# Kernel optimization log

Hardware: AMD Instinct MI355X
Metric: run time of the kernel (lower is better)

The kernel has to match this reference:

```python
import jax, jax.numpy as jnp
import numpy as np

TOP_K = 2  # moe_top_k


def setup_inputs() -> dict:
    key = jax.random.key(0)
    k0, k1, k2, k3 = jax.random.split(key, 4)
    SL, BS, H, F, E = 2048, 4, 1024, 1024, 8
    x = jax.random.normal(k0, (SL, BS, H), dtype=jnp.float32)
    w_router = jax.random.normal(k1, (H, E), dtype=jnp.float32) * 0.02
    w1 = jax.random.normal(k2, (E, H, F), dtype=jnp.float32) * 0.02  # per-expert map weights
    w2 = jax.random.normal(k3, (E, F, H), dtype=jnp.float32) * 0.02  # per-expert reduce weights
    return {"x": x, "w_router": w_router, "w1": w1, "w2": w2}


def reference(x, w_router, w1, w2):
    # dMoA forward: router -> dropless dispatch -> per-expert map GEMM ->
    # per-expert reduce GEMM -> expert-weighted combine. Dropless = no capacity
    # dropping, so a dense all-experts compute + per-token selection is exactly
    # equivalent in math to the sort/gather/grouped-GEMM/scatter pipeline.
    sl, bs, h = x.shape
    E = w1.shape[0]
    xt = x.reshape(-1, h)  # [T, H], T = sl*bs
    T = xt.shape[0]

    # LearnedRouter: softmax over expert logits, then top-k weights/indices
    scores = jax.nn.softmax(xt @ w_router, axis=-1)       # [T, E]
    expert_weights, top_experts = jax.lax.top_k(scores, TOP_K)  # [T, K]

    # load-balancing loss (router.loss): E * sum_e f_e * p_e
    onehot = jax.nn.one_hot(top_experts, E, dtype=xt.dtype)  # [T, K, E]
    tokens_frac = onehot.sum(axis=(0, 1)) / (T * TOP_K)      # f_e
    probs_mean = scores.mean(axis=0)                         # p_e
    loss = E * jnp.sum(tokens_frac * probs_mean)

    # map: per-expert linear H->F, select the top-k experts' outputs per token
    y_all = jnp.einsum('th,ehf->tef', xt, w1)                 # [T, E, F]
    h_tk = jnp.take_along_axis(y_all, top_experts[:, :, None], axis=1)  # [T, K, F]

    # reduce: weighted scatter-combine, then per-expert linear F->H
    hw = jnp.einsum('tke,tk,tkf->tef', onehot, expert_weights, h_tk)  # [T, E, F]
    out = jnp.einsum('tef,efh->th', hw, w2)                   # [T, H]
    return out.reshape(sl, bs, h), loss
```

## Files before the change

### kernel.cpp

```cpp
#include <hip/hip_runtime.h>
#include <hip/hip_bf16.h>
#include <stdint.h>


#define HD 1024
#define FD 1024
#define EN 8

typedef __attribute__((ext_vector_type(8))) short bf16x8;
typedef __attribute__((ext_vector_type(4))) float f32x4;

__device__ __forceinline__ void gload16(const void* g, void* l) {
    __builtin_amdgcn_global_load_lds(
        (const __attribute__((address_space(1))) unsigned int*)g,
        (__attribute__((address_space(3))) unsigned int*)l, 16, 0, 0);
}

__device__ __forceinline__ ushort f2bf(float v) {
    __hip_bfloat16 h = __float2bfloat16(v);
    return *(ushort*)&h;
}
__device__ __forceinline__ float bf2f(ushort u) {
    unsigned int w = ((unsigned int)u) << 16;
    float f; __builtin_memcpy(&f, &w, 4); return f;
}

__global__ __launch_bounds__(256) void router_kernel(
    const float* __restrict__ x, const float* __restrict__ wrt,
    ushort* __restrict__ xb,
    int* __restrict__ top_e, float* __restrict__ top_w,
    int* __restrict__ counts, float* __restrict__ probsum)
{
    __shared__ int   cnt_s[EN];
    __shared__ float ps_s[EN];
    int tid = threadIdx.x;
    if (tid < EN) { cnt_s[tid] = 0; ps_s[tid] = 0.f; }
    __syncthreads();

    int wid = tid >> 6, lane = tid & 63;
    int t = blockIdx.x * 4 + wid;
    const float4* xr4 = (const float4*)(x + (size_t)t * HD);
    ushort4* xbo = (ushort4*)(xb + (size_t)t * HD);
    float acc[EN];
#pragma unroll
    for (int e = 0; e < EN; e++) acc[e] = 0.f;
#pragma unroll
    for (int it = 0; it < 4; it++) {
        float4 xv = xr4[it * 64 + lane];
        ushort4 o; o.x = f2bf(xv.x); o.y = f2bf(xv.y); o.z = f2bf(xv.z); o.w = f2bf(xv.w);
        xbo[it * 64 + lane] = o;
        int h0 = it * 256 + lane * 4;
        float xs[4] = {xv.x, xv.y, xv.z, xv.w};
#pragma unroll
        for (int j = 0; j < 4; j++) {
            const float4* wp = (const float4*)(wrt + (size_t)(h0 + j) * EN);
            float4 wa = wp[0], wb = wp[1];
            acc[0] += xs[j] * wa.x; acc[1] += xs[j] * wa.y;
            acc[2] += xs[j] * wa.z; acc[3] += xs[j] * wa.w;
            acc[4] += xs[j] * wb.x; acc[5] += xs[j] * wb.y;
            acc[6] += xs[j] * wb.z; acc[7] += xs[j] * wb.w;
        }
    }
#pragma unroll
    for (int off = 32; off >= 1; off >>= 1) {
#pragma unroll
        for (int e = 0; e < EN; e++) acc[e] += __shfl_xor(acc[e], off, 64);
    }
    if (lane == 0) {
        float m = acc[0];
#pragma unroll
        for (int e = 1; e < EN; e++) m = fmaxf(m, acc[e]);
        float p[EN], s = 0.f;
#pragma unroll
        for (int e = 0; e < EN; e++) { p[e] = expf(acc[e] - m); s += p[e]; }
        float inv = 1.f / s;
#pragma unroll
        for (int e = 0; e < EN; e++) p[e] *= inv;
        int e0 = 0;
#pragma unroll
        for (int e = 1; e < EN; e++) if (p[e] > p[e0]) e0 = e;
        int e1 = (e0 == 0) ? 1 : 0;
#pragma unroll
        for (int e = 0; e < EN; e++) {
            if (e == e0) continue;
            if (p[e] > p[e1]) e1 = e;
        }
        top_e[t * 2] = e0;  top_e[t * 2 + 1] = e1;
        top_w[t * 2] = p[e0]; top_w[t * 2 + 1] = p[e1];
        atomicAdd(&cnt_s[e0], 1); atomicAdd(&cnt_s[e1], 1);
#pragma unroll
        for (int e = 0; e < EN; e++) atomicAdd(&ps_s[e], p[e]);
    }
    __syncthreads();
    if (tid < EN) {
        atomicAdd(&counts[tid], cnt_s[tid]);
        atomicAdd(&probsum[tid], ps_s[tid]);
    }
}

__global__ void prep_kernel(const int* __restrict__ counts,
                            const float* __restrict__ probsum,
                            int* __restrict__ offs, float* __restrict__ loss_out)
{
    int off = 0; float loss = 0.f;
    for (int e = 0; e < EN; e++) {
        offs[e] = off;
        off += counts[e];
        loss += ((float)counts[e] / 16384.f) * (probsum[e] / 8192.f);
    }
    offs[EN] = off;
    *loss_out = 8.f * loss;
}

__global__ __launch_bounds__(256) void dispatch_kernel(
    const int* __restrict__ top_e, const float* __restrict__ top_w,
    const int* __restrict__ offs, int* __restrict__ cursor,
    int* __restrict__ tok_list, float* __restrict__ w_list)
{
    int t = blockIdx.x * 256 + threadIdx.x;
    int lane = threadIdx.x & 63;
#pragma unroll
    for (int k = 0; k < 2; k++) {
        int e = top_e[t * 2 + k];
        int idx = 0;
#pragma unroll
        for (int ex = 0; ex < EN; ex++) {
            unsigned long long m = __ballot(e == ex);
            if (e == ex) {
                int cnt = __popcll(m);
                int leader = __ffsll(m) - 1;
                int pos = 0;
                if (lane == leader) pos = atomicAdd(&cursor[ex * 16], cnt);
                pos = __shfl(pos, leader, 64);
                int rank = __popcll(m & ((1ull << lane) - 1ull));
                idx = offs[ex] + pos + rank;
            }
        }
        tok_list[idx] = t * 2 + k;
        w_list[idx] = top_w[t * 2 + k];
    }
}

__global__ __launch_bounds__(256) void transpose_conv_kernel(
    const float* __restrict__ w1, const float* __restrict__ w2,
    ushort* __restrict__ w1b, ushort* __restrict__ w2b)
{
    __shared__ float tile[32][33];
    int bid = blockIdx.x;
    const float* in; ushort* outp;
    if (bid >= 8192) { in = w2; outp = w2b; bid -= 8192; }
    else             { in = w1; outp = w1b; }
    int e  = bid >> 10;
    int t2 = bid & 1023;
    int tb = t2 >> 5;
    int ta = t2 & 31;
    const float* pin = in + ((size_t)e << 20);
    ushort* pout = outp + ((size_t)e << 20);
    int tx = threadIdx.x & 31, ty = threadIdx.x >> 5;
#pragma unroll
    for (int j = 0; j < 4; j++)
        tile[ty + j * 8][tx] = pin[(size_t)(ta * 32 + ty + j * 8) * 1024 + tb * 32 + tx];
    __syncthreads();
#pragma unroll
    for (int j = 0; j < 4; j++)
        pout[(size_t)(tb * 32 + ty + j * 8) * 1024 + ta * 32 + tx] =
            f2bf(tile[tx][ty + j * 8]);
}


__global__ __launch_bounds__(512, 2) void map_gemm(
    const ushort* __restrict__ xb, const ushort* __restrict__ w1b,
    ushort* __restrict__ hbuf,
    const int* __restrict__ tok_list, const float* __restrict__ w_list,
    const int* __restrict__ offs)
{
    __shared__ __align__(16) short lA[2][256][64];
    __shared__ __align__(16) short lB[2][256][64];
    __shared__ int   tok_s[256];
    __shared__ float wt_s[256];

    int g = blockIdx.x;
    int e = g & 7, q = g >> 3, nb = q & 3, rb = q >> 2;
    int base = offs[e], cnt = offs[e + 1] - base;
    int row0 = rb << 8;
    if (row0 >= cnt) return;
    int rem = cnt - row0;
    int tid = threadIdx.x;
    if (tid < 256) {
        int r = row0 + tid; if (r > cnt - 1) r = cnt - 1;
        tok_s[tid] = tok_list[base + r];
        wt_s[tid]  = w_list[base + r];
    }
    __syncthreads();

    int lane = tid & 63, w = tid >> 6;
    int wm = w >> 2, wn = w & 3;
    int w32 = w * 32;
    int lr = lane >> 3;
    int kseg = ((lane & 7) ^ lr) << 3;

    const ushort* pA[4]; const ushort* pB[4];
    const ushort* wbase = w1b + ((size_t)e << 20);
#pragma unroll
    for (int i = 0; i < 4; i++) {
        int rowT = w32 + i * 8 + lr;
        pA[i] = xb + (size_t)(tok_s[rowT] >> 1) * HD + kseg;
        pB[i] = wbase + (size_t)(nb * 256 + rowT) * HD + kseg;
    }

    f32x4 acc[8][4];
#pragma unroll
    for (int m = 0; m < 8; m++)
#pragma unroll
        for (int n = 0; n < 4; n++) acc[m][n] = (f32x4){0.f, 0.f, 0.f, 0.f};

#pragma unroll
    for (int i = 0; i < 4; i++) {
        gload16(pA[i], &lA[0][w32 + i * 8][0]);
        gload16(pB[i], &lB[0][w32 + i * 8][0]);
        pA[i] += 64; pB[i] += 64;
    }

    int lo = lane & 15, hi = lane >> 4, rx = lane & 7;
    for (int t = 0; t < 16; ++t) {
        int cur = t & 1;
        if (t < 15) {
            int nxt = cur ^ 1;
#pragma unroll
            for (int i = 0; i < 4; i++) {
                gload16(pA[i], &lA[nxt][w32 + i * 8][0]);
                gload16(pB[i], &lB[nxt][w32 + i * 8][0]);
                pA[i] += 64; pB[i] += 64;
            }
            asm volatile("s_waitcnt vmcnt(8)" ::: "memory");
        } else {
            asm volatile("s_waitcnt vmcnt(0)" ::: "memory");
        }
        __builtin_amdgcn_s_barrier();
        __builtin_amdgcn_sched_barrier(0);

        __builtin_amdgcn_s_setprio(1);
#pragma unroll
        for (int ks = 0; ks < 2; ks++) {
            bf16x8 af[8], bg[4];
#pragma unroll
            for (int m = 0; m < 8; m++)
                af[m] = *(const bf16x8*)&lA[cur][wm * 128 + m * 16 + lo][((ks * 4 + hi) ^ rx) << 3];
#pragma unroll
            for (int n = 0; n < 4; n++)
                bg[n] = *(const bf16x8*)&lB[cur][wn * 64 + n * 16 + lo][((ks * 4 + hi) ^ rx) << 3];
#pragma unroll
            for (int m = 0; m < 8; m++)
#pragma unroll
                for (int n = 0; n < 4; n++)
                    acc[m][n] = __builtin_amdgcn_mfma_f32_16x16x32_bf16(af[m], bg[n], acc[m][n], 0, 0, 0);
        }
        __builtin_amdgcn_s_setprio(0);
        __builtin_amdgcn_sched_barrier(0);
        asm volatile("s_waitcnt lgkmcnt(0)" ::: "memory");
        __builtin_amdgcn_s_barrier();
        __builtin_amdgcn_sched_barrier(0);
    }

    short* ep = (w < 4 ? (short*)lA : (short*)lB) + (w & 3) * 8192;
#pragma unroll
    for (int m = 0; m < 8; m++)
#pragma unroll
        for (int r = 0; r < 4; r++) {
            int row_l = m * 16 + hi * 4 + r;
            int rswz = (row_l & 7) << 4;
            float wgt = wt_s[wm * 128 + row_l];
#pragma unroll
            for (int n = 0; n < 4; n++) {
                int colb = (n * 16 + lo) * 2;
                ep[(row_l * 128 + (colb ^ rswz)) >> 1] = f2bf(acc[m][n][r] * wgt);
            }
        }
    __syncthreads();
    size_t outbase = (size_t)(base + row0);
    int colg0 = (nb << 8) + wn * 64;
#pragma unroll
    for (int j = 0; j < 16; j++) {
        int row_l = j * 8 + (lane >> 3);
        int r_blk = wm * 128 + row_l;
        int sb = ((lane & 7) * 16) ^ ((row_l & 7) << 4);
        bf16x8 v = *(const bf16x8*)&ep[(row_l * 128 + sb) >> 1];
        if (r_blk < rem)
            *(bf16x8*)&hbuf[(outbase + r_blk) * FD + colg0 + (lane & 7) * 8] = v;
    }
}

__global__ __launch_bounds__(512, 2) void reduce_gemm(
    const ushort* __restrict__ hbuf, const ushort* __restrict__ w2b,
    ushort* __restrict__ obuf,
    const int* __restrict__ tok_list, const int* __restrict__ offs)
{
    __shared__ __align__(16) short lA[2][256][64];
    __shared__ __align__(16) short lB[2][256][64];
    __shared__ int tok_s[256];

    int g = blockIdx.x;
    int e = g & 7, q = g >> 3, nb = q & 3, rb = q >> 2;
    int base = offs[e], cnt = offs[e + 1] - base;
    int row0 = rb << 8;
    if (row0 >= cnt) return;
    int rem = cnt - row0;
    int tid = threadIdx.x;
    if (tid < 256) {
        int r = row0 + tid; if (r > cnt - 1) r = cnt - 1;
        tok_s[tid] = tok_list[base + r];
    }
    __syncthreads();

    int lane = tid & 63, w = tid >> 6;
    int wm = w >> 2, wn = w & 3;
    int w32 = w * 32;
    int lr = lane >> 3;
    int kseg = ((lane & 7) ^ lr) << 3;

    const ushort* pA[4]; const ushort* pB[4];
    const ushort* wbase = w2b + ((size_t)e << 20);
#pragma unroll
    for (int i = 0; i < 4; i++) {
        int rowT = w32 + i * 8 + lr;
        int ar = row0 + rowT; if (ar > cnt - 1) ar = cnt - 1;
        pA[i] = hbuf + (size_t)(base + ar) * FD + kseg;
        pB[i] = wbase + (size_t)(nb * 256 + rowT) * FD + kseg;
    }

    f32x4 acc[8][4];
#pragma unroll
    for (int m = 0; m < 8; m++)
#pragma unroll
        for (int n = 0; n < 4; n++) acc[m][n] = (f32x4){0.f, 0.f, 0.f, 0.f};

#pragma unroll
    for (int i = 0; i < 4; i++) {
        gload16(pA[i], &lA[0][w32 + i * 8][0]);
        gload16(pB[i], &lB[0][w32 + i * 8][0]);
        pA[i] += 64; pB[i] += 64;
    }

    int lo = lane & 15, hi = lane >> 4, rx = lane & 7;
    for (int t = 0; t < 16; ++t) {
        int cur = t & 1;
        if (t < 15) {
            int nxt = cur ^ 1;
#pragma unroll
            for (int i = 0; i < 4; i++) {
                gload16(pA[i], &lA[nxt][w32 + i * 8][0]);
                gload16(pB[i], &lB[nxt][w32 + i * 8][0]);
                pA[i] += 64; pB[i] += 64;
            }
            asm volatile("s_waitcnt vmcnt(8)" ::: "memory");
        } else {
            asm volatile("s_waitcnt vmcnt(0)" ::: "memory");
        }
        __builtin_amdgcn_s_barrier();
        __builtin_amdgcn_sched_barrier(0);

        __builtin_amdgcn_s_setprio(1);
#pragma unroll
        for (int ks = 0; ks < 2; ks++) {
            bf16x8 af[8], bg[4];
#pragma unroll
            for (int m = 0; m < 8; m++)
                af[m] = *(const bf16x8*)&lA[cur][wm * 128 + m * 16 + lo][((ks * 4 + hi) ^ rx) << 3];
#pragma unroll
            for (int n = 0; n < 4; n++)
                bg[n] = *(const bf16x8*)&lB[cur][wn * 64 + n * 16 + lo][((ks * 4 + hi) ^ rx) << 3];
#pragma unroll
            for (int m = 0; m < 8; m++)
#pragma unroll
                for (int n = 0; n < 4; n++)
                    acc[m][n] = __builtin_amdgcn_mfma_f32_16x16x32_bf16(af[m], bg[n], acc[m][n], 0, 0, 0);
        }
        __builtin_amdgcn_s_setprio(0);
        __builtin_amdgcn_sched_barrier(0);
        asm volatile("s_waitcnt lgkmcnt(0)" ::: "memory");
        __builtin_amdgcn_s_barrier();
        __builtin_amdgcn_sched_barrier(0);
    }

    short* ep = (w < 4 ? (short*)lA : (short*)lB) + (w & 3) * 8192;
#pragma unroll
    for (int m = 0; m < 8; m++)
#pragma unroll
        for (int r = 0; r < 4; r++) {
            int row_l = m * 16 + hi * 4 + r;
            int rswz = (row_l & 7) << 4;
#pragma unroll
            for (int n = 0; n < 4; n++) {
                int colb = (n * 16 + lo) * 2;
                ep[(row_l * 128 + (colb ^ rswz)) >> 1] = f2bf(acc[m][n][r]);
            }
        }
    __syncthreads();
    int colg0 = (nb << 8) + wn * 64;
#pragma unroll
    for (int j = 0; j < 16; j++) {
        int row_l = j * 8 + (lane >> 3);
        int r_blk = wm * 128 + row_l;
        int sb = ((lane & 7) * 16) ^ ((row_l & 7) << 4);
        bf16x8 v = *(const bf16x8*)&ep[(row_l * 128 + sb) >> 1];
        if (r_blk < rem)
            *(bf16x8*)&obuf[(size_t)tok_s[r_blk] * HD + colg0 + (lane & 7) * 8] = v;
    }
}

__global__ __launch_bounds__(256) void combine_kernel(
    const ushort* __restrict__ obuf, float* __restrict__ out)
{
    int g = blockIdx.x * 256 + threadIdx.x;
    int t = g >> 7, c8 = (g & 127) << 3;
    const ushort* p = obuf + (size_t)t * 2048 + c8;
    bf16x8 a = *(const bf16x8*)p;
    bf16x8 b = *(const bf16x8*)(p + 1024);
    float o[8];
#pragma unroll
    for (int i = 0; i < 8; i++)
        o[i] = bf2f((ushort)a[i]) + bf2f((ushort)b[i]);
    float* q = out + (size_t)t * HD + c8;
    *(float4*)q       = (float4){o[0], o[1], o[2], o[3]};
    *(float4*)(q + 4) = (float4){o[4], o[5], o[6], o[7]};
}

extern "C" void kernel_launch(void* const* d_in, const int* in_sizes, int n_in,
                              void* d_out, int out_size, void* d_ws, size_t ws_size,
                              hipStream_t stream)
{
    const float* x   = (const float*)d_in[0];
    const float* wrt = (const float*)d_in[1];
    const float* w1  = (const float*)d_in[2];
    const float* w2  = (const float*)d_in[3];
    float* out = (float*)d_out;

    uint8_t* ws = (uint8_t*)d_ws;
    ushort* xb   = (ushort*)(ws);
    ushort* w1b  = (ushort*)(ws + (16u << 20));
    ushort* obuf = (ushort*)(ws);
    ushort* w2b  = (ushort*)(ws + (32u << 20));
    ushort* hbuf = (ushort*)(ws + (48u << 20));
    uint8_t* p80 = ws + (80u << 20);
    int*   tok_list = (int*)(p80);
    float* w_list   = (float*)(p80 + (64u << 10));
    int*   top_e    = (int*)(p80 + (128u << 10));
    float* top_w    = (float*)(p80 + (192u << 10));
    uint8_t* ctr    = p80 + (256u << 10);
    int*   counts   = (int*)(ctr);
    float* probsum  = (float*)(ctr + 64);
    int*   offs     = (int*)(ctr + 128);
    int*   cursor   = (int*)(ctr + 256);
    float* loss_out = out + 8388608;

    hipMemsetAsync(ctr, 0, 1024, stream);

    router_kernel<<<2048, 256, 0, stream>>>(x, wrt, xb, top_e, top_w, counts, probsum);
    prep_kernel<<<1, 1, 0, stream>>>(counts, probsum, offs, loss_out);
    dispatch_kernel<<<32, 256, 0, stream>>>(top_e, top_w, offs, cursor, tok_list, w_list);
    transpose_conv_kernel<<<16384, 256, 0, stream>>>(w1, w2, w1b, w2b);
    map_gemm<<<1024, 512, 0, stream>>>(xb, w1b, hbuf, tok_list, w_list, offs);
    reduce_gemm<<<1024, 512, 0, stream>>>(hbuf, w2b, obuf, tok_list, offs);
    combine_kernel<<<4096, 256, 0, stream>>>(obuf, out);
}
```

Baseline: 227.9 us.

## Interleave LDS reads, global prefetch and MFMA quadrants in grouped GEMM main loops

Both expert GEMM main loops now split each k-tile's 8x4 MFMA block into four quadrants. LDS fragment reads, via inline ds_read_b128, and the next-tile global-to-LDS loads are spread between the quadrants, so fragment register pressure drops and memory issue overlaps with matrix math. The per-iteration sync now waits for vmcnt(0) at the loop end instead of vmcnt(8) at the top. This trades some prefetch depth for a finer interleave, and the extra waits may expose more latency.

```diff
diff --git a/kernel.cpp b/kernel.cpp
--- a/kernel.cpp
+++ b/kernel.cpp
@@ -14,6 +14,14 @@
     __builtin_amdgcn_global_load_lds(
         (const __attribute__((address_space(1))) unsigned int*)g,
         (__attribute__((address_space(3))) unsigned int*)l, 16, 0, 0);
+}
+
+__device__ __forceinline__ bf16x8 ds_read128(const short* p) {
+    bf16x8 r;
+    asm volatile("ds_read_b128 %0, %1"
+                 : "=v"(r)
+                 : "v"((const __attribute__((address_space(3))) short*)p));
+    return r;
 }
 
 __device__ __forceinline__ ushort f2bf(float v) {
@@ -168,6 +176,26 @@
 }
 
 
+#define RDA(ml_, ks_) ds_read128(&lA[cur][wm * 128 + (ml_) * 16 + lo][(((ks_) * 4 + hi) ^ rx) << 3])
+#define RDB(n_, ks_)  ds_read128(&lB[cur][wn * 64  + (n_) * 16 + lo][(((ks_) * 4 + hi) ^ rx) << 3])
+#define MFMA_Q(mb_, nb_)                                                      \
+    do {                                                                      \
+        _Pragma("unroll") for (int ks = 0; ks < 2; ks++)                      \
+        _Pragma("unroll") for (int ml = 0; ml < 4; ml++)                      \
+        _Pragma("unroll") for (int nl = 0; nl < 2; nl++)                      \
+            acc[(mb_) + ml][(nb_) + nl] =                                     \
+                __builtin_amdgcn_mfma_f32_16x16x32_bf16(                      \
+                    a[ml][ks], b[(nb_) + nl][ks], acc[(mb_) + ml][(nb_) + nl],\
+                    0, 0, 0);                                                 \
+    } while (0)
+#define LGK0_FENCE()                                                          \
+    do { asm volatile("s_waitcnt lgkmcnt(0)");                                \
+         __builtin_amdgcn_sched_barrier(0); } while (0)
+#define BOUNDARY()                                                            \
+    do { asm volatile("s_waitcnt vmcnt(0)" ::: "memory");                     \
+         __builtin_amdgcn_s_barrier();                                        \
+         __builtin_amdgcn_sched_barrier(0); } while (0)
+
 __global__ __launch_bounds__(512, 2) void map_gemm(
     const ushort* __restrict__ xb, const ushort* __restrict__ w1b,
     ushort* __restrict__ hbuf,
@@ -220,46 +248,61 @@
         gload16(pB[i], &lB[0][w32 + i * 8][0]);
         pA[i] += 64; pB[i] += 64;
     }
+    BOUNDARY();
 
     int lo = lane & 15, hi = lane >> 4, rx = lane & 7;
+    bf16x8 a[4][2], b[4][2];
+
     for (int t = 0; t < 16; ++t) {
-        int cur = t & 1;
-        if (t < 15) {
-            int nxt = cur ^ 1;
-#pragma unroll
-            for (int i = 0; i < 4; i++) {
-                gload16(pA[i], &lA[nxt][w32 + i * 8][0]);
-                gload16(pB[i], &lB[nxt][w32 + i * 8][0]);
-                pA[i] += 64; pB[i] += 64;
-            }
-            asm volatile("s_waitcnt vmcnt(8)" ::: "memory");
-        } else {
-            asm volatile("s_waitcnt vmcnt(0)" ::: "memory");
-        }
-        __builtin_amdgcn_s_barrier();
-        __builtin_amdgcn_sched_barrier(0);
-
-        __builtin_amdgcn_s_setprio(1);
+        int cur = t & 1, nxt = cur ^ 1;
+        bool pf = (t < 15);
 #pragma unroll
         for (int ks = 0; ks < 2; ks++) {
-            bf16x8 af[8], bg[4];
-#pragma unroll
-            for (int m = 0; m < 8; m++)
-                af[m] = *(const bf16x8*)&lA[cur][wm * 128 + m * 16 + lo][((ks * 4 + hi) ^ rx) << 3];
-#pragma unroll
-            for (int n = 0; n < 4; n++)
-                bg[n] = *(const bf16x8*)&lB[cur][wn * 64 + n * 16 + lo][((ks * 4 + hi) ^ rx) << 3];
-#pragma unroll
-            for (int m = 0; m < 8; m++)
-#pragma unroll
-                for (int n = 0; n < 4; n++)
-                    acc[m][n] = __builtin_amdgcn_mfma_f32_16x16x32_bf16(af[m], bg[n], acc[m][n], 0, 0, 0);
-        }
-        __builtin_amdgcn_s_setprio(0);
-        __builtin_amdgcn_sched_barrier(0);
-        asm volatile("s_waitcnt lgkmcnt(0)" ::: "memory");
-        __builtin_amdgcn_s_barrier();
-        __builtin_amdgcn_sched_barrier(0);
+            a[0][ks] = RDA(0, ks); a[1][ks] = RDA(1, ks);
+            a[2][ks] = RDA(2, ks); a[3][ks] = RDA(3, ks);
+            b[0][ks] = RDB(0, ks); b[1][ks] = RDB(1, ks);
+        }
+        if (pf) {
+            gload16(pA[0], &lA[nxt][w32 + 0][0]);  pA[0] += 64;
+            gload16(pB[0], &lB[nxt][w32 + 0][0]);  pB[0] += 64;
+            gload16(pA[1], &lA[nxt][w32 + 8][0]);  pA[1] += 64;
+            gload16(pB[1], &lB[nxt][w32 + 8][0]);  pB[1] += 64;
+        }
+        LGK0_FENCE();
+        __builtin_amdgcn_s_setprio(1);
+        MFMA_Q(0, 0);
+        __builtin_amdgcn_s_setprio(0);
+        __builtin_amdgcn_sched_barrier(0);
+#pragma unroll
+        for (int ks = 0; ks < 2; ks++) {
+            b[2][ks] = RDB(2, ks); b[3][ks] = RDB(3, ks);
+        }
+        if (pf) {
+            gload16(pA[2], &lA[nxt][w32 + 16][0]); pA[2] += 64;
+            gload16(pB[2], &lB[nxt][w32 + 16][0]); pB[2] += 64;
+            gload16(pA[3], &lA[nxt][w32 + 24][0]); pA[3] += 64;
+            gload16(pB[3], &lB[nxt][w32 + 24][0]); pB[3] += 64;
+        }
+        LGK0_FENCE();
+        __builtin_amdgcn_s_setprio(1);
+        MFMA_Q(0, 2);
+        __builtin_amdgcn_s_setprio(0);
+        __builtin_amdgcn_sched_barrier(0);
+#pragma unroll
+        for (int ks = 0; ks < 2; ks++) {
+            a[0][ks] = RDA(4, ks); a[1][ks] = RDA(5, ks);
+            a[2][ks] = RDA(6, ks); a[3][ks] = RDA(7, ks);
+        }
+        LGK0_FENCE();
+        __builtin_amdgcn_s_setprio(1);
+        MFMA_Q(4, 2);
+        __builtin_amdgcn_s_setprio(0);
+        __builtin_amdgcn_sched_barrier(0);
+        __builtin_amdgcn_s_setprio(1);
+        MFMA_Q(4, 0);
+        __builtin_amdgcn_s_setprio(0);
+        __builtin_amdgcn_sched_barrier(0);
+        BOUNDARY();
     }
 
     short* ep = (w < 4 ? (short*)lA : (short*)lB) + (w & 3) * 8192;
@@ -340,46 +383,61 @@
         gload16(pB[i], &lB[0][w32 + i * 8][0]);
         pA[i] += 64; pB[i] += 64;
     }
+    BOUNDARY();
 
     int lo = lane & 15, hi = lane >> 4, rx = lane & 7;
+    bf16x8 a[4][2], b[4][2];
+
     for (int t = 0; t < 16; ++t) {
-        int cur = t & 1;
-        if (t < 15) {
-            int nxt = cur ^ 1;
-#pragma unroll
-            for (int i = 0; i < 4; i++) {
-                gload16(pA[i], &lA[nxt][w32 + i * 8][0]);
-                gload16(pB[i], &lB[nxt][w32 + i * 8][0]);
-                pA[i] += 64; pB[i] += 64;
-            }
-            asm volatile("s_waitcnt vmcnt(8)" ::: "memory");
-        } else {
-            asm volatile("s_waitcnt vmcnt(0)" ::: "memory");
-        }
-        __builtin_amdgcn_s_barrier();
-        __builtin_amdgcn_sched_barrier(0);
-
-        __builtin_amdgcn_s_setprio(1);
+        int cur = t & 1, nxt = cur ^ 1;
+        bool pf = (t < 15);
 #pragma unroll
         for (int ks = 0; ks < 2; ks++) {
-            bf16x8 af[8], bg[4];
-#pragma unroll
-            for (int m = 0; m < 8; m++)
-                af[m] = *(const bf16x8*)&lA[cur][wm * 128 + m * 16 + lo][((ks * 4 + hi) ^ rx) << 3];
-#pragma unroll
-            for (int n = 0; n < 4; n++)
-                bg[n] = *(const bf16x8*)&lB[cur][wn * 64 + n * 16 + lo][((ks * 4 + hi) ^ rx) << 3];
-#pragma unroll
-            for (int m = 0; m < 8; m++)
-#pragma unroll
-                for (int n = 0; n < 4; n++)
-                    acc[m][n] = __builtin_amdgcn_mfma_f32_16x16x32_bf16(af[m], bg[n], acc[m][n], 0, 0, 0);
-        }
-        __builtin_amdgcn_s_setprio(0);
-        __builtin_amdgcn_sched_barrier(0);
-        asm volatile("s_waitcnt lgkmcnt(0)" ::: "memory");
-        __builtin_amdgcn_s_barrier();
-        __builtin_amdgcn_sched_barrier(0);
+            a[0][ks] = RDA(0, ks); a[1][ks] = RDA(1, ks);
+            a[2][ks] = RDA(2, ks); a[3][ks] = RDA(3, ks);
+            b[0][ks] = RDB(0, ks); b[1][ks] = RDB(1, ks);
+        }
+        if (pf) {
+            gload16(pA[0], &lA[nxt][w32 + 0][0]);  pA[0] += 64;
+            gload16(pB[0], &lB[nxt][w32 + 0][0]);  pB[0] += 64;
+            gload16(pA[1], &lA[nxt][w32 + 8][0]);  pA[1] += 64;
+            gload16(pB[1], &lB[nxt][w32 + 8][0]);  pB[1] += 64;
+        }
+        LGK0_FENCE();
+        __builtin_amdgcn_s_setprio(1);
+        MFMA_Q(0, 0);
+        __builtin_amdgcn_s_setprio(0);
+        __builtin_amdgcn_sched_barrier(0);
+#pragma unroll
+        for (int ks = 0; ks < 2; ks++) {
+            b[2][ks] = RDB(2, ks); b[3][ks] = RDB(3, ks);
+        }
+        if (pf) {
+            gload16(pA[2], &lA[nxt][w32 + 16][0]); pA[2] += 64;
+            gload16(pB[2], &lB[nxt][w32 + 16][0]); pB[2] += 64;
+            gload16(pA[3], &lA[nxt][w32 + 24][0]); pA[3] += 64;
+            gload16(pB[3], &lB[nxt][w32 + 24][0]); pB[3] += 64;
+        }
+        LGK0_FENCE();
+        __builtin_amdgcn_s_setprio(1);
+        MFMA_Q(0, 2);
+        __builtin_amdgcn_s_setprio(0);
+        __builtin_amdgcn_sched_barrier(0);
+#pragma unroll
+        for (int ks = 0; ks < 2; ks++) {
+            a[0][ks] = RDA(4, ks); a[1][ks] = RDA(5, ks);
+            a[2][ks] = RDA(6, ks); a[3][ks] = RDA(7, ks);
+        }
+        LGK0_FENCE();
+        __builtin_amdgcn_s_setprio(1);
+        MFMA_Q(4, 2);
+        __builtin_amdgcn_s_setprio(0);
+        __builtin_amdgcn_sched_barrier(0);
+        __builtin_amdgcn_s_setprio(1);
+        MFMA_Q(4, 0);
+        __builtin_amdgcn_s_setprio(0);
+        __builtin_amdgcn_sched_barrier(0);
+        BOUNDARY();
     }
 
     short* ep = (w < 4 ? (short*)lA : (short*)lB) + (w & 3) * 8192;
```

Measured after the change: 205.1 us. 10.0% less time.
